# Kernel optimization log

Hardware: AMD Instinct MI355X
Metric: run time of the kernel (lower is better)

The kernel has to match this reference:

```python
import jax, jax.numpy as jnp
import numpy as np

B, C, H, W = 4, 8, 384, 384
NUM_LAYERS = 5
CG_ITERS = 10


def conv2d(x, w, b):
    # x: [B,Cin,H,W], w: [Cout,Cin,3,3]
    y = jax.lax.conv_general_dilated(x, w, (1, 1), 'SAME',
                                     dimension_numbers=('NCHW', 'OIHW', 'NCHW'))
    return y + b[None, :, None, None]


def dw(x, w_in, b_in, ws_mid, bs_mid, w_out, b_out):
    # Sequence: conv, conv, relu, conv, conv, relu, conv, conv, relu, conv, conv, relu, conv
    h = conv2d(x, w_in, b_in)
    for i in range(7):
        h = conv2d(h, ws_mid[i], bs_mid[i])
        if i % 2 == 0:  # ReLU after convs 2,4,6,8
            h = jax.nn.relu(h)
    h = conv2d(h, w_out, b_out)
    return x + h  # residual


def conjugate_grad(rhs, csm_c, mask, lam):
    # rhs: [B,H,W] complex; csm_c: [B,C,H,W] complex; mask: [B,H,W] real
    def AtA(p):
        coil = csm_c * p[:, None]                      # [B,C,H,W]
        k = jnp.fft.fft2(coil) * mask[:, None]         # masked k-space
        return jnp.sum(jnp.conj(csm_c) * jnp.fft.ifft2(k), axis=1)

    def body(carry, _):
        x, r, p, rTr = carry
        Ap = AtA(p) + lam * p
        pAp = jnp.sum(jnp.conj(p) * Ap, axis=(-2, -1)).real
        alpha = rTr / pAp
        x = x + alpha[:, None, None] * p
        r = r - alpha[:, None, None] * Ap
        rTrNew = jnp.sum(jnp.conj(r) * r, axis=(-2, -1)).real
        beta = rTrNew / rTr
        p = r + beta[:, None, None] * p
        return (x, r, p, rTrNew), None

    x0 = jnp.zeros_like(rhs)
    rTr0 = jnp.sum(jnp.conj(rhs) * rhs, axis=(-2, -1)).real
    (x, _, _, _), _ = jax.lax.scan(body, (x0, rhs, rhs, rTr0), None, length=CG_ITERS)
    return x


def reference(under_img, csm, mask, lam, w_in, b_in, ws_mid, bs_mid, w_out, b_out):
    csm_c = jax.lax.complex(csm[..., 0], csm[..., 1])  # [B,C,H,W] complex
    lam_s = lam[0]
    x = under_img
    for _ in range(NUM_LAYERS):
        x = dw(x, w_in, b_in, ws_mid, bs_mid, w_out, b_out)
        x = under_img + lam_s * x
        rhs = jax.lax.complex(x[:, 0], x[:, 1])        # view_as_complex(permute(0,2,3,1))
        xc = conjugate_grad(rhs, csm_c, mask, lam_s)
        x = jnp.stack([xc.real, xc.imag], axis=1)      # view_as_real -> [B,2,H,W]
    return x


def setup_inputs() -> dict:
    key = jax.random.key(0)
    ks = jax.random.split(key, 8)
    under_img = jax.random.normal(ks[0], (B, 2, H, W), jnp.float32)
    csm = jax.random.normal(ks[1], (B, C, H, W, 2), jnp.float32) / np.sqrt(C)
    mask = (jax.random.uniform(ks[2], (B, H, W)) > 0.5).astype(jnp.float32)
    lam = jnp.array([0.05], jnp.float32)
    w_in = jax.random.normal(ks[3], (64, 2, 3, 3), jnp.float32) * 0.02
    b_in = jnp.zeros((64,), jnp.float32)
    ws_mid = jax.random.normal(ks[4], (7, 64, 64, 3, 3), jnp.float32) * 0.02
    bs_mid = jnp.zeros((7, 64), jnp.float32)
    w_out = jax.random.normal(ks[5], (2, 64, 3, 3), jnp.float32) * 0.02
    b_out = jnp.zeros((2,), jnp.float32)
    return {"under_img": under_img, "csm": csm, "mask": mask, "lam": lam,
            "w_in": w_in, "b_in": b_in, "ws_mid": ws_mid, "bs_mid": bs_mid,
            "w_out": w_out, "b_out": b_out}
```

## Files before the change

kernel.cpp:

```cpp
#include <hip/hip_runtime.h>
#include <hip/hip_bf16.h>
#include <math.h>

#define HH 384
#define WW 384
#define HW (HH*WW)
#define BB 4
#define CC 8
#define NLAYERS 5
#define CGITERS 10
#define PI_F 3.14159265358979323846f

typedef __attribute__((ext_vector_type(8))) short short8;
typedef __attribute__((ext_vector_type(4))) float floatx4;

struct cf { float x, y; };
__device__ __forceinline__ cf cadd(cf a, cf b){ cf r; r.x=a.x+b.x; r.y=a.y+b.y; return r; }
__device__ __forceinline__ cf csub(cf a, cf b){ cf r; r.x=a.x-b.x; r.y=a.y-b.y; return r; }
__device__ __forceinline__ cf cmul(cf a, cf b){ cf r; r.x=a.x*b.x - a.y*b.y; r.y=a.x*b.y + a.y*b.x; return r; }
__device__ __forceinline__ cf csqr(cf a){ cf r; r.x = a.x*a.x - a.y*a.y; r.y = 2.f*a.x*a.y; return r; }
__device__ __forceinline__ cf shflxor(cf v, int m){ cf r; r.x = __shfl_xor(v.x, m); r.y = __shfl_xor(v.y, m); return r; }
__device__ __forceinline__ int brev7(int l){ return (int)(__brev((unsigned)l) >> 25); }
__device__ __forceinline__ int padi(int i){ return i + (i >> 3); }

__device__ __forceinline__ void radix3(cf a0, cf a1, cf a2, float s3, cf y[3]) {
  float tx = a1.x + a2.x, ty_ = a1.y + a2.y;
  float ux = a1.x - a2.x, uy = a1.y - a2.y;
  y[0].x = a0.x + tx;              y[0].y = a0.y + ty_;
  y[1].x = a0.x - 0.5f*tx - s3*uy; y[1].y = a0.y - 0.5f*ty_ + s3*ux;
  y[2].x = a0.x - 0.5f*tx + s3*uy; y[2].y = a0.y - 0.5f*ty_ - s3*ux;
}

template<int SIGN>
__device__ __forceinline__ void fft384_wave(int l, const cf v[6], cf uA[3], cf uB[3]) {
  const float s3 = SIGN * 0.8660254037844386f;
  radix3(v[0], v[2], v[4], s3, uA);
  radix3(v[1], v[3], v[5], s3, uB);
  float sA, cA;
  __sincosf(SIGN * (2.0f * PI_F / 384.0f) * (float)l, &sA, &cA);
  cf wA1; wA1.x = cA; wA1.y = sA;
  cf wA2 = csqr(wA1);
  cf w6; w6.x = 0.5f; w6.y = s3;
  cf wB1 = cmul(wA1, w6);
  cf wB2 = csqr(wB1);
  uA[1] = cmul(uA[1], wA1); uA[2] = cmul(uA[2], wA2);
  uB[1] = cmul(uB[1], wB1); uB[2] = cmul(uB[2], wB2);
  cf u = cmul(wA2, wA1);
  #pragma unroll
  for (int k1 = 0; k1 < 3; ++k1) {
    cf a = uA[k1], b = uB[k1];
    uA[k1] = cadd(a, b);
    uB[k1] = cmul(csub(a, b), u);
  }
  #pragma unroll
  for (int h = 32; h >= 1; h >>= 1) {
    u = csqr(u);
    const bool up = (l & h) != 0;
    #pragma unroll
    for (int k1 = 0; k1 < 3; ++k1) {
      cf pa = shflxor(uA[k1], h);
      cf pb = shflxor(uB[k1], h);
      cf na = up ? cmul(csub(uA[k1], pa), u) : cadd(uA[k1], pa);
      cf nb = up ? cmul(csub(uB[k1], pb), u) : cadd(uB[k1], pb);
      uA[k1] = na; uB[k1] = nb;
    }
  }
}


__global__ void repack_mid_k(const float* __restrict__ ws_mid, __hip_bfloat16* __restrict__ wrep) {
  const int idx = blockIdx.x * 256 + threadIdx.x;
  if (idx >= 7*9*64*64) return;
  const int ci = idx & 63, co = (idx >> 6) & 63, tap = (idx >> 12) % 9, i = idx / (9*4096);
  wrep[idx] = __float2bfloat16(ws_mid[(((size_t)i*64 + co)*64 + ci)*9 + tap]);
}

__global__ void __launch_bounds__(256) conv_in_k(const float* __restrict__ xin,
                                                 const float* __restrict__ w,
                                                 const float* __restrict__ bias,
                                                 __hip_bfloat16* __restrict__ out) {
  __shared__ float tile[2][340];
  const int tx = threadIdx.x & 31, ty = threadIdx.x >> 5;
  const int x0 = blockIdx.x * 32, y0 = blockIdx.y * 8, b = blockIdx.z;
  for (int e = threadIdx.x; e < 680; e += 256) {
    int ci = e / 340, rr = e % 340;
    int iy = y0 - 1 + rr / 34, ix = x0 - 1 + rr % 34;
    float v = 0.f;
    if (iy >= 0 && iy < HH && ix >= 0 && ix < WW)
      v = xin[(b*2 + ci)*HW + iy*WW + ix];
    tile[ci][rr] = v;
  }
  __syncthreads();
  float acc[64];
  #pragma unroll
  for (int co = 0; co < 64; ++co) acc[co] = bias[co];
  #pragma unroll
  for (int ci = 0; ci < 2; ++ci) {
    float v0 = tile[ci][ty*34+tx],     v1 = tile[ci][ty*34+tx+1],     v2 = tile[ci][ty*34+tx+2];
    float v3 = tile[ci][(ty+1)*34+tx], v4 = tile[ci][(ty+1)*34+tx+1], v5 = tile[ci][(ty+1)*34+tx+2];
    float v6 = tile[ci][(ty+2)*34+tx], v7 = tile[ci][(ty+2)*34+tx+1], v8 = tile[ci][(ty+2)*34+tx+2];
    #pragma unroll
    for (int co = 0; co < 64; ++co) {
      const float* wp = w + co*18 + ci*9;
      float a = acc[co];
      a = fmaf(v0, wp[0], a); a = fmaf(v1, wp[1], a); a = fmaf(v2, wp[2], a);
      a = fmaf(v3, wp[3], a); a = fmaf(v4, wp[4], a); a = fmaf(v5, wp[5], a);
      a = fmaf(v6, wp[6], a); a = fmaf(v7, wp[7], a); a = fmaf(v8, wp[8], a);
      acc[co] = a;
    }
  }
  const size_t obase = ((size_t)(b*HH + y0 + ty)*WW + (x0 + tx))*64;
  #pragma unroll
  for (int s = 0; s < 8; ++s) {
    uint4 u;
    __hip_bfloat16* hp = (__hip_bfloat16*)&u;
    #pragma unroll
    for (int j = 0; j < 8; ++j) hp[j] = __float2bfloat16(acc[s*8 + j]);
    *(uint4*)(out + obase + s*8) = u;
  }
}

__global__ void __launch_bounds__(256) conv_mid_mfma_k(
    const __hip_bfloat16* __restrict__ in,
    const __hip_bfloat16* __restrict__ wrep,
    const float* __restrict__ bias,
    __hip_bfloat16* __restrict__ out, int relu) {
  __shared__ __align__(16) __hip_bfloat16 atile[340*64];
  const int tid = threadIdx.x;
  const int l = tid & 63, wv = tid >> 6;
  const int x0 = blockIdx.x * 32, y0 = blockIdx.y * 8, b = blockIdx.z;

  const int kseg = l >> 4;
  const int lr = l & 15;

  const __hip_bfloat16* wlane = wrep + lr*64 + kseg*8;
  short8 bf[4][2];
  #pragma unroll
  for (int nt = 0; nt < 4; ++nt) {
    bf[nt][0] = *(const short8*)(wlane + nt*1024);
    bf[nt][1] = *(const short8*)(wlane + nt*1024 + 32);
  }

  const bool interior = (blockIdx.x >= 1) && (blockIdx.x <= 10) &&
                        (blockIdx.y >= 1) && (blockIdx.y <= 46);
  if (interior) {
    const __hip_bfloat16* inb = in + (size_t)b*HW*64;
    #pragma unroll
    for (int i = 0; i < 10; ++i) {
      const int j = i*256 + tid;
      const int p = j >> 3, s = j & 7;
      const int iy = y0 - 1 + p / 34, ix = x0 - 1 + p % 34;
      const int g = s ^ (p & 7);
      const __hip_bfloat16* src = inb + ((size_t)iy*WW + ix)*64 + g*8;
      __builtin_amdgcn_global_load_lds(
          (const __attribute__((address_space(1))) void*)src,
          (__attribute__((address_space(3))) void*)(atile + (i*256 + wv*64)*8),
          16, 0, 0);
    }
    if (tid < 160) {
      const int j = 2560 + tid;
      const int p = j >> 3, s = j & 7;
      const int iy = y0 - 1 + p / 34, ix = x0 - 1 + p % 34;
      const int g = s ^ (p & 7);
      uint4 v = *(const uint4*)(inb + ((size_t)iy*WW + ix)*64 + g*8);
      *(uint4*)(atile + j*8) = v;
    }
  } else {
    for (int e = tid; e < 2720; e += 256) {
      const int p = e >> 3, s = e & 7;
      const int iy = y0 - 1 + p / 34, ix = x0 - 1 + p % 34;
      const int g = s ^ (p & 7);
      uint4 v = make_uint4(0u, 0u, 0u, 0u);
      if (iy >= 0 && iy < HH && ix >= 0 && ix < WW)
        v = *(const uint4*)(in + ((size_t)(b*HH + iy)*WW + ix)*64 + g*8);
      *(uint4*)(atile + e*8) = v;
    }
  }

  floatx4 acc[4][4];
  #pragma unroll
  for (int mt = 0; mt < 4; ++mt)
    #pragma unroll
    for (int nt = 0; nt < 4; ++nt)
      acc[mt][nt] = (floatx4){0.f, 0.f, 0.f, 0.f};

  __syncthreads();

  #pragma unroll 1
  for (int tap = 0; tap < 9; ++tap) {
    short8 bfn[4][2];
    if (tap < 8) {
      const __hip_bfloat16* wn = wlane + (tap + 1)*4096;
      #pragma unroll
      for (int nt = 0; nt < 4; ++nt) {
        bfn[nt][0] = *(const short8*)(wn + nt*1024);
        bfn[nt][1] = *(const short8*)(wn + nt*1024 + 32);
      }
    }
    const int dy = tap / 3, dx = tap - dy*3;
    short8 af[4][2];
    #pragma unroll
    for (int mt = 0; mt < 4; ++mt) {
      const int ry = 2*wv + (mt >> 1) + dy;
      const int px = (mt & 1)*16 + lr + dx;
      const int p  = ry*34 + px;
      const int eo = p*64 + ((kseg ^ (p & 7)) << 3);
      af[mt][0] = *(const short8*)(atile + eo);
      af[mt][1] = *(const short8*)(atile + (eo ^ 32));
    }
    #pragma unroll
    for (int mt = 0; mt < 4; ++mt)
      #pragma unroll
      for (int nt = 0; nt < 4; ++nt) {
        acc[mt][nt] = __builtin_amdgcn_mfma_f32_16x16x32_bf16(af[mt][0], bf[nt][0], acc[mt][nt], 0, 0, 0);
        acc[mt][nt] = __builtin_amdgcn_mfma_f32_16x16x32_bf16(af[mt][1], bf[nt][1], acc[mt][nt], 0, 0, 0);
      }
    if (tap < 8) {
      #pragma unroll
      for (int nt = 0; nt < 4; ++nt) { bf[nt][0] = bfn[nt][0]; bf[nt][1] = bfn[nt][1]; }
    }
  }

  __syncthreads();
  __hip_bfloat16* otile = atile;
  #pragma unroll
  for (int mt = 0; mt < 4; ++mt) {
    const int row = 2*wv + (mt >> 1);
    #pragma unroll
    for (int nt = 0; nt < 4; ++nt) {
      const int ch = nt*16 + lr;
      const float bv = bias[ch];
      #pragma unroll
      for (int rr = 0; rr < 4; ++rr) {
        const int px = (mt & 1)*16 + kseg*4 + rr;
        float v = acc[mt][nt][rr] + bv;
        if (relu) v = fmaxf(v, 0.f);
        otile[(row*32 + px)*72 + ch] = __float2bfloat16(v);
      }
    }
  }
  __syncthreads();
  #pragma unroll
  for (int iter = 0; iter < 8; ++iter) {
    const int p = iter*32 + (tid >> 3), s = tid & 7;
    const int row = p >> 5, px = p & 31;
    uint4 v = *(const uint4*)(&otile[p*72 + s*8]);
    *(uint4*)(out + ((size_t)(b*HH + y0 + row)*WW + (x0 + px))*64 + s*8) = v;
  }
}

__global__ void __launch_bounds__(256) conv_out_k(const __hip_bfloat16* __restrict__ in,
                                                  const float* __restrict__ w,
                                                  const float* __restrict__ bias,
                                                  const float* __restrict__ xcur,
                                                  const float* __restrict__ under,
                                                  const float* __restrict__ lam,
                                                  cf* __restrict__ r, cf* __restrict__ p,
                                                  cf* __restrict__ xc, float* __restrict__ scL) {
  __shared__ __hip_bfloat16 atile[340*72];
  __shared__ float wl[2*64*9];
  __shared__ float wsum[4];
  const int tid = threadIdx.x;
  const int tx = tid & 31, ty = tid >> 5;
  const int x0 = blockIdx.x * 32, y0 = blockIdx.y * 8, b = blockIdx.z;

  for (int e = tid; e < 340*8; e += 256) {
    int pp = e >> 3, s = e & 7;
    int iy = y0 - 1 + pp / 34, ix = x0 - 1 + pp % 34;
    uint4 v = make_uint4(0u, 0u, 0u, 0u);
    if (iy >= 0 && iy < HH && ix >= 0 && ix < WW)
      v = *(const uint4*)(in + ((size_t)(b*HH + iy)*WW + ix)*64 + s*8);
    *(uint4*)(&atile[pp*72 + s*8]) = v;
  }
  for (int e = tid; e < 2*64*9; e += 256) wl[e] = w[e];
  __syncthreads();

  float a0 = bias[0], a1 = bias[1];
  #pragma unroll 1
  for (int tap = 0; tap < 9; ++tap) {
    const int dy = tap / 3, dx = tap - dy*3;
    const __hip_bfloat16* ap = &atile[((ty + dy)*34 + tx + dx)*72];
    #pragma unroll
    for (int s = 0; s < 8; ++s) {
      short8 v8 = *(const short8*)(ap + s*8);
      const __hip_bfloat16* hv = (const __hip_bfloat16*)&v8;
      #pragma unroll
      for (int j = 0; j < 8; ++j) {
        const float f = __bfloat162float(hv[j]);
        a0 = fmaf(f, wl[(s*8 + j)*9 + tap], a0);
        a1 = fmaf(f, wl[(64 + s*8 + j)*9 + tap], a1);
      }
    }
  }
  const float lamv = lam[0];
  const int y = y0 + ty, x = x0 + tx;
  const int idx2 = y*WW + x;
  float xv0 = xcur[b*2*HW + idx2],  xv1 = xcur[b*2*HW + HW + idx2];
  float u0  = under[b*2*HW + idx2], u1  = under[b*2*HW + HW + idx2];
  float r0 = u0 + lamv * (xv0 + a0);
  float r1 = u1 + lamv * (xv1 + a1);
  const int cidx = b*HW + idx2;
  cf vv; vv.x = r0; vv.y = r1;
  r[cidx] = vv; p[cidx] = vv;
  cf zz; zz.x = 0.f; zz.y = 0.f; xc[cidx] = zz;
  float partial = r0*r0 + r1*r1;
  for (int off = 32; off; off >>= 1) partial += __shfl_down(partial, off);
  const int l = tid & 63, wvid = tid >> 6;
  if (l == 0) wsum[wvid] = partial;
  __syncthreads();
  if (tid == 0) atomicAdd(&scL[b], wsum[0]+wsum[1]+wsum[2]+wsum[3]);
}


__global__ void __launch_bounds__(256) pass_a_k(const cf* __restrict__ rold, cf* __restrict__ rnew,
                                                const cf* __restrict__ pold, cf* __restrict__ pnew,
                                                cf* __restrict__ xc, const cf* __restrict__ Ap,
                                                const cf* __restrict__ csm, cf* __restrict__ t,
                                                float* __restrict__ scL, int it) {
  __shared__ cf rowbuf[4][434];
  const int l = threadIdx.x & 63, wv = threadIdx.x >> 6;
  const int y = blockIdx.x * 4 + wv;
  const int c = blockIdx.y, b = blockIdx.z;
  const int rowoff = b*HW + y*WW;
  cf pv[6];
  if (it == 0) {
    #pragma unroll
    for (int m = 0; m < 6; ++m) pv[m] = pold[rowoff + l + 64*m];
  } else {
    const float rtrp  = scL[(it-1)*4 + b];
    const float pApp  = scL[40 + (it-1)*4 + b];
    const float ApApp = scL[80 + (it-1)*4 + b];
    const float alpha = rtrp / pApp;
    const float rtrn  = alpha*alpha*ApApp - rtrp;
    const float beta  = rtrn / rtrp;
    if (blockIdx.x == 0 && c == 0 && threadIdx.x == 0) scL[it*4 + b] = rtrn;
    #pragma unroll
    for (int m = 0; m < 6; ++m) {
      const int idx = rowoff + l + 64*m;
      cf rv = rold[idx];
      cf av = Ap[idx];
      rv.x -= alpha*av.x; rv.y -= alpha*av.y;
      cf po = pold[idx];
      pv[m].x = rv.x + beta*po.x; pv[m].y = rv.y + beta*po.y;
      if (c == 0) {
        rnew[idx] = rv;
        pnew[idx] = pv[m];
        cf xv = xc[idx]; xv.x += alpha*po.x; xv.y += alpha*po.y; xc[idx] = xv;
      }
    }
  }
  const cf* crow = csm + (b*CC + c)*HW + y*WW;
  cf v[6];
  #pragma unroll
  for (int m = 0; m < 6; ++m) v[m] = cmul(crow[l + 64*m], pv[m]);
  cf uA[3], uB[3];
  fft384_wave<-1>(l, v, uA, uB);
  const int R3 = 3 * brev7(l);
  cf* rb = rowbuf[wv];
  #pragma unroll
  for (int k1 = 0; k1 < 3; ++k1) { rb[padi(k1 + R3)] = uA[k1]; rb[padi(k1 + R3 + 3)] = uB[k1]; }
  cf* trow = t + (b*CC + c)*HW + y*WW;
  #pragma unroll
  for (int m = 0; m < 6; ++m) trow[l + 64*m] = rb[padi(l + 64*m)];
}

__global__ void __launch_bounds__(256) pass_b_k(cf* __restrict__ t, const float* __restrict__ mask) {
  __shared__ cf tile[431*9];
  const int b = blockIdx.z, c = blockIdx.y, x0 = blockIdx.x * 8;
  cf* base = t + (b*CC + c)*HW;
  for (int e = threadIdx.x; e < 3072; e += 256) {
    int y = e >> 3, xx = e & 7;
    tile[padi(y)*9 + xx] = base[y*WW + x0 + xx];
  }
  __syncthreads();
  const int l = threadIdx.x & 63, wv = threadIdx.x >> 6;
  const int R3 = 3 * brev7(l);
  for (int rep = 0; rep < 2; ++rep) {
    const int xx = wv*2 + rep, x = x0 + xx;
    cf v[6];
    #pragma unroll
    for (int m = 0; m < 6; ++m) v[m] = tile[padi(l + 64*m)*9 + xx];
    cf uA[3], uB[3];
    fft384_wave<-1>(l, v, uA, uB);
    const float* mrow = mask + b*HW + x;
    #pragma unroll
    for (int k1 = 0; k1 < 3; ++k1) {
      float mA = mrow[(k1 + R3)*WW], mB = mrow[(k1 + R3 + 3)*WW];
      uA[k1].x *= mA; uA[k1].y *= mA; uB[k1].x *= mB; uB[k1].y *= mB;
    }
    __syncthreads();
    #pragma unroll
    for (int k1 = 0; k1 < 3; ++k1) { tile[padi(k1 + R3)*9 + xx] = uA[k1]; tile[padi(k1 + R3 + 3)*9 + xx] = uB[k1]; }
    __syncthreads();
    #pragma unroll
    for (int m = 0; m < 6; ++m) v[m] = tile[padi(l + 64*m)*9 + xx];
    fft384_wave<1>(l, v, uA, uB);
    const float s = 1.0f / 384.0f;
    #pragma unroll
    for (int k1 = 0; k1 < 3; ++k1) {
      uA[k1].x *= s; uA[k1].y *= s; uB[k1].x *= s; uB[k1].y *= s;
      tile[padi(k1 + R3)*9 + xx] = uA[k1]; tile[padi(k1 + R3 + 3)*9 + xx] = uB[k1];
    }
    __syncthreads();
  }
  for (int e = threadIdx.x; e < 3072; e += 256) {
    int y = e >> 3, xx = e & 7;
    base[y*WW + x0 + xx] = tile[padi(y)*9 + xx];
  }
}

__global__ void __launch_bounds__(256) pass_c_k(const cf* __restrict__ t, const cf* __restrict__ csm,
                                                const cf* __restrict__ p, cf* __restrict__ Ap,
                                                const float* __restrict__ lam,
                                                float* __restrict__ scL, int it) {
  __shared__ cf rowbuf[4][434];
  __shared__ cf redbuf[3][384];
  const int l = threadIdx.x & 63, wv = threadIdx.x >> 6;
  const int y = blockIdx.x, b = blockIdx.y;
  const int R3 = 3 * brev7(l);
  cf* rb = rowbuf[wv];
  cf acc[6] = {};
  #pragma unroll 1
  for (int ci = 0; ci < 2; ++ci) {
    const int c = wv*2 + ci;
    const cf* trow = t + (b*CC + c)*HW + y*WW;
    cf v[6];
    #pragma unroll
    for (int m = 0; m < 6; ++m) v[m] = trow[l + 64*m];
    cf uA[3], uB[3];
    fft384_wave<1>(l, v, uA, uB);
    #pragma unroll
    for (int k1 = 0; k1 < 3; ++k1) { rb[padi(k1 + R3)] = uA[k1]; rb[padi(k1 + R3 + 3)] = uB[k1]; }
    const cf* crow = csm + (b*CC + c)*HW + y*WW;
    #pragma unroll
    for (int m = 0; m < 6; ++m) {
      cf cs = crow[l + 64*m];
      cf wz = rb[padi(l + 64*m)];
      acc[m].x += cs.x*wz.x + cs.y*wz.y;
      acc[m].y += cs.x*wz.y - cs.y*wz.x;
    }
  }
  if (wv > 0) {
    #pragma unroll
    for (int m = 0; m < 6; ++m) redbuf[wv - 1][l + 64*m] = acc[m];
  }
  __syncthreads();
  if (wv == 0) {
    #pragma unroll
    for (int m = 0; m < 6; ++m) {
      #pragma unroll
      for (int j = 0; j < 3; ++j) {
        cf o = redbuf[j][l + 64*m];
        acc[m].x += o.x; acc[m].y += o.y;
      }
    }
    const float lamv = lam[0];
    const float sc384 = 1.0f / 384.0f;
    const cf* prow = p + b*HW + y*WW;
    cf* aprow = Ap + b*HW + y*WW;
    float partial = 0.f, partial2 = 0.f;
    #pragma unroll
    for (int m = 0; m < 6; ++m) {
      cf pv = prow[l + 64*m];
      cf ap; ap.x = acc[m].x*sc384 + lamv*pv.x; ap.y = acc[m].y*sc384 + lamv*pv.y;
      aprow[l + 64*m] = ap;
      partial  += pv.x*ap.x + pv.y*ap.y;
      partial2 += ap.x*ap.x + ap.y*ap.y;
    }
    #pragma unroll
    for (int off = 32; off; off >>= 1) {
      partial  += __shfl_down(partial, off);
      partial2 += __shfl_down(partial2, off);
    }
    if (l == 0) {
      atomicAdd(&scL[40 + it*4 + b], partial);
      atomicAdd(&scL[80 + it*4 + b], partial2);
    }
  }
}

__global__ void __launch_bounds__(256) final_x_k(const cf* __restrict__ xc, const cf* __restrict__ p9,
                                                 const float* __restrict__ scL, float* __restrict__ out) {
  const int idx = blockIdx.x * 256 + threadIdx.x;
  const int b = idx / HW;
  const int rem = idx - b*HW;
  const float alpha = scL[(CGITERS-1)*4 + b] / scL[40 + (CGITERS-1)*4 + b];
  cf xv = xc[idx], pv = p9[idx];
  xv.x += alpha*pv.x; xv.y += alpha*pv.y;
  out[b*2*HW + rem] = xv.x;
  out[b*2*HW + HW + rem] = xv.y;
}

__global__ void zero_sc_k(float* sc) {
  for (int i = threadIdx.x; i < NLAYERS*128; i += 256) sc[i] = 0.f;
}

extern "C" void kernel_launch(void* const* d_in, const int* in_sizes, int n_in,
                              void* d_out, int out_size, void* d_ws, size_t ws_size,
                              hipStream_t stream) {
  (void)in_sizes; (void)n_in; (void)out_size; (void)ws_size;
  const float* under  = (const float*)d_in[0];
  const cf*    csm    = (const cf*)d_in[1];
  const float* mask   = (const float*)d_in[2];
  const float* lam    = (const float*)d_in[3];
  const float* w_in   = (const float*)d_in[4];
  const float* b_in   = (const float*)d_in[5];
  const float* ws_mid = (const float*)d_in[6];
  const float* bs_mid = (const float*)d_in[7];
  const float* w_out  = (const float*)d_in[8];
  const float* b_out  = (const float*)d_in[9];
  float* xcur = (float*)d_out;

  char* bws = (char*)d_ws;
  size_t off = 0;
  auto carve = [&](size_t bytes) { char* pp = bws + off; off += (bytes + 255) & ~(size_t)255; return (void*)pp; };
  __hip_bfloat16* actA = (__hip_bfloat16*)carve((size_t)BB*64*HW*2);
  __hip_bfloat16* actB = (__hip_bfloat16*)carve((size_t)BB*64*HW*2);
  cf* t     = (cf*)carve((size_t)BB*CC*HW*8);
  cf* rbuf0 = (cf*)carve((size_t)BB*HW*8);
  cf* rbuf1 = (cf*)carve((size_t)BB*HW*8);
  cf* pbuf0 = (cf*)carve((size_t)BB*HW*8);
  cf* pbuf1 = (cf*)carve((size_t)BB*HW*8);
  cf* xc    = (cf*)carve((size_t)BB*HW*8);
  cf* Ap    = (cf*)carve((size_t)BB*HW*8);
  float* sc = (float*)carve(4096);
  __hip_bfloat16* wrep = (__hip_bfloat16*)carve((size_t)7*9*64*64*2);

  hipMemcpyAsync(xcur, under, (size_t)BB*2*HW*sizeof(float), hipMemcpyDeviceToDevice, stream);

  zero_sc_k<<<1, 256, 0, stream>>>(sc);
  repack_mid_k<<<(7*9*64*64 + 255)/256, 256, 0, stream>>>(ws_mid, wrep);

  dim3 cgrid(WW/32, HH/8, BB);
  dim3 agrid(HH/4, CC, BB);
  dim3 bgrid(WW/8, CC, BB);
  dim3 c2grid(HH, BB);
  const int egrid = BB*HW/256;

  __hip_bfloat16* bufs[2] = { actA, actB };
  cf* rb[2] = { rbuf0, rbuf1 };
  cf* pb[2] = { pbuf0, pbuf1 };

  for (int layer = 0; layer < NLAYERS; ++layer) {
    float* scL = sc + layer*128;
    conv_in_k<<<cgrid, 256, 0, stream>>>(xcur, w_in, b_in, bufs[0]);
    for (int i = 0; i < 7; ++i) {
      conv_mid_mfma_k<<<cgrid, 256, 0, stream>>>(bufs[i & 1], wrep + (size_t)i*9*4096,
                                                 bs_mid + i*64, bufs[(i + 1) & 1], (i % 2 == 0) ? 1 : 0);
    }
    conv_out_k<<<cgrid, 256, 0, stream>>>(bufs[1], w_out, b_out, xcur, under, lam,
                                          rbuf0, pbuf0, xc, scL);
    for (int it = 0; it < CGITERS; ++it) {
      cf* rold = rb[(it + 1) & 1];
      cf* rnew = rb[it & 1];
      cf* pold = pb[(it + 1) & 1];
      cf* pnew = pb[it & 1];
      if (it == 0) { rold = rbuf0; pold = pbuf0; rnew = rbuf0; pnew = pbuf0; }
      pass_a_k<<<agrid, 256, 0, stream>>>(rold, rnew, pold, pnew, xc, Ap, csm, t, scL, it);
      pass_b_k<<<bgrid, 256, 0, stream>>>(t, mask);
      pass_c_k<<<c2grid, 256, 0, stream>>>(t, csm, pnew, Ap, lam, scL, it);
    }
    final_x_k<<<egrid, 256, 0, stream>>>(xc, pb[(CGITERS - 1) & 1], scL, xcur);
  }
}
```

Before: 9.453 ms.

## Pad activation buffers with zero halo and enlarge mid-conv tiles to 32x16

Activation buffers are stored with a one-pixel zero border (386x386), written once by a new guard-zeroing kernel, so the conv kernels can drop boundary checks and every mid-conv block can use the async global-to-LDS load path. The mid-layer MFMA conv now runs 512-thread blocks covering 16 rows instead of 8, which cuts the redundant halo loads per output. In exchange it uses more LDS per block and more registers per thread, which may lower occupancy, and the parts of the kernel not shown must agree with the new 8-wave tiling.

After: 10.86 ms. 1.15x slower.

```diff
diff --git a/kernel.cpp b/kernel.cpp
--- a/kernel.cpp
+++ b/kernel.cpp
@@ -5,6 +5,8 @@
 #define HH 384
 #define WW 384
 #define HW (HH*WW)
+#define WP 386
+#define PP (386*386)
 #define BB 4
 #define CC 8
 #define NLAYERS 5
@@ -75,6 +77,20 @@
   wrep[idx] = __float2bfloat16(ws_mid[(((size_t)i*64 + co)*64 + ci)*9 + tap]);
 }
 
+__global__ void zero_guard_k(__hip_bfloat16* __restrict__ a, __hip_bfloat16* __restrict__ b2) {
+  const int idx = blockIdx.x * 256 + threadIdx.x;
+  if (idx >= 2*BB*1540*8) return;
+  const int s = idx & 7; int rest = idx >> 3;
+  const int px = rest % 1540; rest /= 1540;
+  const int bb = rest & 3; const int buf = rest >> 2;
+  int row, col;
+  if (px < WP)        { row = 0;    col = px; }
+  else if (px < 2*WP) { row = HH+1; col = px - WP; }
+  else { const int k = px - 2*WP; row = 1 + (k >> 1); col = (k & 1) ? (WW+1) : 0; }
+  __hip_bfloat16* base = buf ? b2 : a;
+  *(uint4*)(base + ((size_t)bb*PP + (size_t)row*WP + col)*64 + s*8) = make_uint4(0u,0u,0u,0u);
+}
+
 __global__ void __launch_bounds__(256) conv_in_k(const float* __restrict__ xin,
                                                  const float* __restrict__ w,
                                                  const float* __restrict__ bias,
@@ -109,7 +125,7 @@
       acc[co] = a;
     }
   }
-  const size_t obase = ((size_t)(b*HH + y0 + ty)*WW + (x0 + tx))*64;
+  const size_t obase = ((size_t)b*PP + (size_t)(y0 + ty + 1)*WP + (x0 + tx + 1))*64;
   #pragma unroll
   for (int s = 0; s < 8; ++s) {
     uint4 u;
@@ -120,15 +136,15 @@
   }
 }
 
-__global__ void __launch_bounds__(256) conv_mid_mfma_k(
+__global__ void __launch_bounds__(512, 4) conv_mid_mfma_k(
     const __hip_bfloat16* __restrict__ in,
     const __hip_bfloat16* __restrict__ wrep,
     const float* __restrict__ bias,
     __hip_bfloat16* __restrict__ out, int relu) {
-  __shared__ __align__(16) __hip_bfloat16 atile[340*64];
+  __shared__ __align__(16) __hip_bfloat16 atile[612*64];
   const int tid = threadIdx.x;
   const int l = tid & 63, wv = tid >> 6;
-  const int x0 = blockIdx.x * 32, y0 = blockIdx.y * 8, b = blockIdx.z;
+  const int x0 = blockIdx.x * 32, y0 = blockIdx.y * 16, b = blockIdx.z;
 
   const int kseg = l >> 4;
   const int lr = l & 15;
@@ -141,40 +157,24 @@
     bf[nt][1] = *(const short8*)(wlane + nt*1024 + 32);
   }
 
-  const bool interior = (blockIdx.x >= 1) && (blockIdx.x <= 10) &&
-                        (blockIdx.y >= 1) && (blockIdx.y <= 46);
-  if (interior) {
-    const __hip_bfloat16* inb = in + (size_t)b*HW*64;
-    #pragma unroll
-    for (int i = 0; i < 10; ++i) {
-      const int j = i*256 + tid;
-      const int p = j >> 3, s = j & 7;
-      const int iy = y0 - 1 + p / 34, ix = x0 - 1 + p % 34;
-      const int g = s ^ (p & 7);
-      const __hip_bfloat16* src = inb + ((size_t)iy*WW + ix)*64 + g*8;
-      __builtin_amdgcn_global_load_lds(
-          (const __attribute__((address_space(1))) void*)src,
-          (__attribute__((address_space(3))) void*)(atile + (i*256 + wv*64)*8),
-          16, 0, 0);
-    }
-    if (tid < 160) {
-      const int j = 2560 + tid;
-      const int p = j >> 3, s = j & 7;
-      const int iy = y0 - 1 + p / 34, ix = x0 - 1 + p % 34;
-      const int g = s ^ (p & 7);
-      uint4 v = *(const uint4*)(inb + ((size_t)iy*WW + ix)*64 + g*8);
-      *(uint4*)(atile + j*8) = v;
-    }
-  } else {
-    for (int e = tid; e < 2720; e += 256) {
-      const int p = e >> 3, s = e & 7;
-      const int iy = y0 - 1 + p / 34, ix = x0 - 1 + p % 34;
-      const int g = s ^ (p & 7);
-      uint4 v = make_uint4(0u, 0u, 0u, 0u);
-      if (iy >= 0 && iy < HH && ix >= 0 && ix < WW)
-        v = *(const uint4*)(in + ((size_t)(b*HH + iy)*WW + ix)*64 + g*8);
-      *(uint4*)(atile + e*8) = v;
-    }
+  const __hip_bfloat16* inb = in + (size_t)b*PP*64;
+  #pragma unroll
+  for (int i = 0; i < 9; ++i) {
+    const int j = i*512 + tid;
+    const int p = j >> 3, s = j & 7;
+    const int g = s ^ (p & 7);
+    const __hip_bfloat16* src = inb + ((size_t)(y0 + p/34)*WP + (x0 + p%34))*64 + g*8;
+    __builtin_amdgcn_global_load_lds(
+        (const __attribute__((address_space(1))) void*)src,
+        (__attribute__((address_space(3))) void*)(atile + (i*512 + wv*64)*8),
+        16, 0, 0);
+  }
+  if (tid < 288) {
+    const int j = 4608 + tid;
+    const int p = j >> 3, s = j & 7;
+    const int g = s ^ (p & 7);
+    uint4 v = *(const uint4*)(inb + ((size_t)(y0 + p/34)*WP + (x0 + p%34))*64 + g*8);
+    *(uint4*)(atile + (size_t)j*8) = v;
   }
 
   floatx4 acc[4][4];
@@ -242,10 +242,10 @@
   __syncthreads();
   #pragma unroll
   for (int iter = 0; iter < 8; ++iter) {
-    const int p = iter*32 + (tid >> 3), s = tid & 7;
+    const int p = iter*64 + (tid >> 3), s = tid & 7;
     const int row = p >> 5, px = p & 31;
     uint4 v = *(const uint4*)(&otile[p*72 + s*8]);
-    *(uint4*)(out + ((size_t)(b*HH + y0 + row)*WW + (x0 + px))*64 + s*8) = v;
+    *(uint4*)(out + ((size_t)b*PP + (size_t)(y0 + row + 1)*WP + (x0 + px + 1))*64 + s*8) = v;
   }
 }
 
@@ -266,10 +266,7 @@
 
   for (int e = tid; e < 340*8; e += 256) {
     int pp = e >> 3, s = e & 7;
-    int iy = y0 - 1 + pp / 34, ix = x0 - 1 + pp % 34;
-    uint4 v = make_uint4(0u, 0u, 0u, 0u);
-    if (iy >= 0 && iy < HH && ix >= 0 && ix < WW)
-      v = *(const uint4*)(in + ((size_t)(b*HH + iy)*WW + ix)*64 + s*8);
+    uint4 v = *(const uint4*)(in + ((size_t)b*PP + (size_t)(y0 + pp/34)*WP + (x0 + pp%34))*64 + s*8);
     *(uint4*)(&atile[pp*72 + s*8]) = v;
   }
   for (int e = tid; e < 2*64*9; e += 256) wl[e] = w[e];
@@ -514,8 +511,8 @@
   char* bws = (char*)d_ws;
   size_t off = 0;
   auto carve = [&](size_t bytes) { char* pp = bws + off; off += (bytes + 255) & ~(size_t)255; return (void*)pp; };
-  __hip_bfloat16* actA = (__hip_bfloat16*)carve((size_t)BB*64*HW*2);
-  __hip_bfloat16* actB = (__hip_bfloat16*)carve((size_t)BB*64*HW*2);
+  __hip_bfloat16* actA = (__hip_bfloat16*)carve((size_t)BB*PP*64*2);
+  __hip_bfloat16* actB = (__hip_bfloat16*)carve((size_t)BB*PP*64*2);
   cf* t     = (cf*)carve((size_t)BB*CC*HW*8);
   cf* rbuf0 = (cf*)carve((size_t)BB*HW*8);
   cf* rbuf1 = (cf*)carve((size_t)BB*HW*8);
@@ -530,8 +527,10 @@
 
   zero_sc_k<<<1, 256, 0, stream>>>(sc);
   repack_mid_k<<<(7*9*64*64 + 255)/256, 256, 0, stream>>>(ws_mid, wrep);
+  zero_guard_k<<<(2*BB*1540*8 + 255)/256, 256, 0, stream>>>(actA, actB);
 
   dim3 cgrid(WW/32, HH/8, BB);
+  dim3 cmgrid(WW/32, HH/16, BB);
   dim3 agrid(HH/4, CC, BB);
   dim3 bgrid(WW/8, CC, BB);
   dim3 c2grid(HH, BB);
@@ -545,8 +544,8 @@
     float* scL = sc + layer*128;
     conv_in_k<<<cgrid, 256, 0, stream>>>(xcur, w_in, b_in, bufs[0]);
     for (int i = 0; i < 7; ++i) {
-      conv_mid_mfma_k<<<cgrid, 256, 0, stream>>>(bufs[i & 1], wrep + (size_t)i*9*4096,
-                                                 bs_mid + i*64, bufs[(i + 1) & 1], (i % 2 == 0) ? 1 : 0);
+      conv_mid_mfma_k<<<cmgrid, 512, 0, stream>>>(bufs[i & 1], wrep + (size_t)i*9*4096,
+                                                  bs_mid + i*64, bufs[(i + 1) & 1], (i % 2 == 0) ? 1 : 0);
     }
     conv_out_k<<<cgrid, 256, 0, stream>>>(bufs[1], w_out, b_out, xcur, under, lam,
                                           rbuf0, pbuf0, xc, scL);
```
